# Kernel optimization log

Hardware: AMD Instinct MI355X
Metric: run time of the kernel (lower is better)

The kernel has to match this reference:

```python
import jax, jax.numpy as jnp
import numpy as np

T, D, H, V, Z = 32, 128, 256, 32000, 256


def _gru_cell(x, h, W_ih, W_hh, b_ih, b_hh):
    # PyTorch GRU cell, gate order r,z,n. x,h: [D,H]
    gi = x @ W_ih.T + b_ih
    gh = h @ W_hh.T + b_hh
    i_r, i_z, i_n = jnp.split(gi, 3, axis=-1)
    h_r, h_z, h_n = jnp.split(gh, 3, axis=-1)
    r = jax.nn.sigmoid(i_r + h_r)
    z = jax.nn.sigmoid(i_z + h_z)
    n = jnp.tanh(i_n + r * h_n)
    return (1.0 - z) * n + z * h


def _tree_rnn(nodes, edges, h0, emb, pc, ps):
    # nodes/edges: [T,D]; h0: [D,H]. Child vs sibling GRU chosen per-node by edges.
    def step(h, te):
        tok, e = te
        x = emb[tok]                       # [D,H]
        hc = _gru_cell(x, h, *pc)
        hs = _gru_cell(x, h, *ps)
        hn = jnp.where(e[:, None], hc, hs)  # branch-aware state update
        return hn, hn                       # seq_len=1, L=1 => output == new state
    h_final, outs = jax.lax.scan(step, h0, (nodes, edges))
    return outs, h_final                    # outs: [T,D,H]


def setup_inputs() -> dict:
    key = jax.random.key(0)
    ks = iter(jax.random.split(key, 48))
    s = 0.05
    def gru():
        return (jax.random.normal(next(ks), (3 * H, H), jnp.float32) * s,
                jax.random.normal(next(ks), (3 * H, H), jnp.float32) * s,
                jnp.zeros((3 * H,), jnp.float32),
                jnp.zeros((3 * H,), jnp.float32))
    inp = {}
    inp['nodes'] = jax.random.randint(next(ks), (T, D), 0, V, dtype=jnp.int32)
    inp['edges'] = jax.random.bernoulli(next(ks), 0.5, (T, D))
    inp['emb'] = jax.random.normal(next(ks), (V, H), jnp.float32) * s
    (inp['enc_c_Wih'], inp['enc_c_Whh'], inp['enc_c_bih'], inp['enc_c_bhh']) = gru()
    (inp['enc_s_Wih'], inp['enc_s_Whh'], inp['enc_s_bih'], inp['enc_s_bhh']) = gru()
    (inp['dec_c_Wih'], inp['dec_c_Whh'], inp['dec_c_bih'], inp['dec_c_bhh']) = gru()
    (inp['dec_s_Wih'], inp['dec_s_Whh'], inp['dec_s_bih'], inp['dec_s_bhh']) = gru()
    inp['W_mean'] = jax.random.normal(next(ks), (Z, H), jnp.float32) * s
    inp['b_mean'] = jnp.zeros((Z,), jnp.float32)
    inp['W_logv'] = jax.random.normal(next(ks), (Z, H), jnp.float32) * s
    inp['b_logv'] = jnp.zeros((Z,), jnp.float32)
    inp['W_l2h'] = jax.random.normal(next(ks), (H, Z), jnp.float32) * s
    inp['b_l2h'] = jnp.zeros((H,), jnp.float32)
    inp['W_out'] = jax.random.normal(next(ks), (V, H), jnp.float32) * s
    inp['b_out'] = jnp.zeros((V,), jnp.float32)
    inp['enc_init'] = jax.random.normal(next(ks), (D, H), jnp.float32) * 0.001
    inp['eps'] = jax.random.normal(next(ks), (D, Z), jnp.float32)
    return inp


def reference(nodes, edges, emb,
              enc_c_Wih, enc_c_Whh, enc_c_bih, enc_c_bhh,
              enc_s_Wih, enc_s_Whh, enc_s_bih, enc_s_bhh,
              dec_c_Wih, dec_c_Whh, dec_c_bih, dec_c_bhh,
              dec_s_Wih, dec_s_Whh, dec_s_bih, dec_s_bhh,
              W_mean, b_mean, W_logv, b_logv, W_l2h, b_l2h,
              W_out, b_out, enc_init, eps):
    pc_e = (enc_c_Wih, enc_c_Whh, enc_c_bih, enc_c_bhh)
    ps_e = (enc_s_Wih, enc_s_Whh, enc_s_bih, enc_s_bhh)
    pc_d = (dec_c_Wih, dec_c_Whh, dec_c_bih, dec_c_bhh)
    ps_d = (dec_s_Wih, dec_s_Whh, dec_s_bih, dec_s_bhh)

    _, hid = _tree_rnn(nodes, edges, enc_init, emb, pc_e, ps_e)  # [D,H]
    mean = hid @ W_mean.T + b_mean                               # [D,Z]
    logv = hid @ W_logv.T + b_logv
    z = eps * jnp.exp(0.5 * logv) + mean                          # reparameterize
    h0 = z @ W_l2h.T + b_l2h                                      # [D,H]
    outs, _ = _tree_rnn(nodes, edges, h0, emb, pc_d, ps_d)        # [T,D,H]
    logits = outs @ W_out.T + b_out                               # [T,D,V]
    logp = jax.nn.log_softmax(logits, axis=-1)
    return logp, mean, logv, z
```

## Files before the change

kernel.cpp:

```cpp
#include <hip/hip_runtime.h>
#include <hip/hip_bf16.h>

#define TT 32
#define DD 128
#define HH 256
#define VV 32000
#define ZZ 256
#define NTL 50
#define NBLK 16
#define GHLP 100

typedef __attribute__((ext_vector_type(8))) short bf16x8;
typedef __attribute__((ext_vector_type(4))) float f32x4;
typedef __attribute__((ext_vector_type(8))) _Float16 f16x8;

static __device__ inline unsigned short f2bf(float x) {
    __hip_bfloat16 h = __float2bfloat16(x);
    return *(unsigned short*)&h;
}

static __device__ inline unsigned long long pack4h(_Float16 a, _Float16 b,
                                                   _Float16 c, _Float16 d) {
    union { _Float16 h[4]; unsigned long long u; } x;
    x.h[0] = a; x.h[1] = b; x.h[2] = c; x.h[3] = d;
    return x.u;
}

__global__ void edge_canon_k(const unsigned char* __restrict__ eb,
                             unsigned char* __restrict__ canon)
{
    __shared__ int flag;
    if (threadIdx.x == 0) flag = 0;
    __syncthreads();
    int acc = 0;
    for (int i = threadIdx.x; i < TT * DD; i += 256)
        if (i & 3) acc |= eb[i];
    if (acc) atomicOr(&flag, 1);
    __syncthreads();
    const bool is_i32 = (flag == 0);
    for (int i = threadIdx.x; i < TT * DD; i += 256)
        canon[i] = is_i32 ? eb[4 * (size_t)i] : eb[i];
}

__global__ __launch_bounds__(256) void pack_frag(
    const float* __restrict__ src, __hip_bfloat16* __restrict__ dst, int nchunks_total)
{
    int i = blockIdx.x * 256 + threadIdx.x;
    if (i >= nchunks_total) return;
    int lane = i & 63, ks = (i >> 6) & 7, j = i >> 9;
    int g = lane >> 4, c = lane & 15;
    const float* s = src + (size_t)(j * 16 + c) * HH + ks * 32 + g * 8;
    float4 v0 = *(const float4*)s;
    float4 v1 = *(const float4*)(s + 4);
    bf16x8 o;
    o[0] = (short)f2bf(v0.x); o[1] = (short)f2bf(v0.y);
    o[2] = (short)f2bf(v0.z); o[3] = (short)f2bf(v0.w);
    o[4] = (short)f2bf(v1.x); o[5] = (short)f2bf(v1.y);
    o[6] = (short)f2bf(v1.z); o[7] = (short)f2bf(v1.w);
    *(bf16x8*)(dst + (size_t)i * 8) = o;
}

__global__ __launch_bounds__(256) void pack_frag4(
    const float* __restrict__ s0, const float* __restrict__ s1,
    const float* __restrict__ s2, const float* __restrict__ s3,
    __hip_bfloat16* __restrict__ dst)
{
    int i = blockIdx.x * 256 + threadIdx.x;
    if (i >= 24576) return;
    int slot = blockIdx.y;
    const float* src = (slot == 0) ? s0 : (slot == 1) ? s1 : (slot == 2) ? s2 : s3;
    __hip_bfloat16* d = dst + (size_t)slot * 196608;
    int lane = i & 63, ks = (i >> 6) & 7, j = i >> 9;
    int g = lane >> 4, c = lane & 15;
    const float* s = src + (size_t)(j * 16 + c) * HH + ks * 32 + g * 8;
    float4 v0 = *(const float4*)s;
    float4 v1 = *(const float4*)(s + 4);
    bf16x8 o;
    o[0] = (short)f2bf(v0.x); o[1] = (short)f2bf(v0.y);
    o[2] = (short)f2bf(v0.z); o[3] = (short)f2bf(v0.w);
    o[4] = (short)f2bf(v1.x); o[5] = (short)f2bf(v1.y);
    o[6] = (short)f2bf(v1.z); o[7] = (short)f2bf(v1.w);
    *(bf16x8*)(d + (size_t)i * 8) = o;
}

__global__ __launch_bounds__(256) void pack_wrnn4(
    const float* __restrict__ s0, const float* __restrict__ s1,
    const float* __restrict__ s2, const float* __restrict__ s3,
    _Float16* __restrict__ dst)
{
    int i = blockIdx.x * 256 + threadIdx.x;
    if (i >= 24576) return;
    int slot = blockIdx.y;
    const float* src = (slot == 0) ? s0 : (slot == 1) ? s1 : (slot == 2) ? s2 : s3;
    _Float16* d = dst + (size_t)slot * 196608;
    int lane = i & 63;
    int t2 = i >> 6;
    int ks = t2 & 7;
    int t3 = t2 >> 3;
    int tt = t3 % 6;
    int j8 = t3 / 6;
    int g = lane >> 4, c = lane & 15;
    int jg2 = tt / 3, gt = tt % 3;
    int srow = gt * 256 + j8 * 32 + jg2 * 16 + c;
    int scol = ks * 32 + g * 8;
    const float* s = src + (size_t)srow * HH + scol;
    float4 v0 = *(const float4*)s;
    float4 v1 = *(const float4*)(s + 4);
    f16x8 o;
    o[0] = (_Float16)v0.x; o[1] = (_Float16)v0.y;
    o[2] = (_Float16)v0.z; o[3] = (_Float16)v0.w;
    o[4] = (_Float16)v1.x; o[5] = (_Float16)v1.y;
    o[6] = (_Float16)v1.z; o[7] = (_Float16)v1.w;
    *(f16x8*)(d + (size_t)i * 8) = o;
}

__global__ __launch_bounds__(256) void gather_pack(
    const int* __restrict__ nodes, const float* __restrict__ emb,
    __hip_bfloat16* __restrict__ dst)
{
    int i = blockIdx.x * 256 + threadIdx.x;
    int lane = i & 63, ks = (i >> 6) & 7, j = i >> 9;
    int g = lane >> 4, c = lane & 15;
    int row = j * 16 + c;
    int tok = nodes[row];
    const float* s = emb + (size_t)tok * HH + ks * 32 + g * 8;
    float4 v0 = *(const float4*)s;
    float4 v1 = *(const float4*)(s + 4);
    bf16x8 o;
    o[0] = (short)f2bf(v0.x); o[1] = (short)f2bf(v0.y);
    o[2] = (short)f2bf(v0.z); o[3] = (short)f2bf(v0.w);
    o[4] = (short)f2bf(v1.x); o[5] = (short)f2bf(v1.y);
    o[6] = (short)f2bf(v1.z); o[7] = (short)f2bf(v1.w);
    *(bf16x8*)(dst + (size_t)i * 8) = o;
}

__global__ __launch_bounds__(256) void pack_lat3(
    const float* __restrict__ s0, const float* __restrict__ s1,
    const float* __restrict__ s2, float* __restrict__ dst)
{
    int i = blockIdx.x * 256 + threadIdx.x;
    int slot = blockIdx.y;
    const float* src = (slot == 0) ? s0 : (slot == 1) ? s1 : s2;
    float* d = dst + (size_t)slot * 65536;
    int j = i & 255, k = i >> 8;
    d[(size_t)k * 256 + j] = src[(size_t)j * 256 + k];
}

template<int MT, bool WRITE_C, bool HAS_BIAS, bool LSE_PARTIAL, bool LSE_SUB>
__global__ __launch_bounds__(256, 2) void gemm_rs(
    const __hip_bfloat16* __restrict__ A,
    const __hip_bfloat16* __restrict__ B,
    int ldc, int nchunks, int ntiles,
    const float* __restrict__ bias,
    const float* __restrict__ lse,
    float* __restrict__ C,
    float* __restrict__ pm, float* __restrict__ ps)
{
    __shared__ float lds_st[WRITE_C ? (4 * 16 * 68) : 1];

    const int tid  = threadIdx.x;
    const int w    = tid >> 6;
    const int lane = tid & 63;
    const int g    = lane >> 4;
    const int c    = lane & 15;
    const int m0   = blockIdx.x * (64 * MT);
    const int n0   = blockIdx.y * (nchunks * 64);
    const int jb0  = n0 >> 4;

    bf16x8 a[MT][8];
#pragma unroll
    for (int mt = 0; mt < MT; ++mt) {
        const int row16 = m0 + mt * 64 + w * 16;
        const __hip_bfloat16* ap = A + (((size_t)(row16 >> 4) * 8) * 64 + lane) * 8;
#pragma unroll
        for (int ks = 0; ks < 8; ++ks) a[mt][ks] = *(const bf16x8*)(ap + ks * 512);
    }

    float mrun[MT][4], srun[MT][4];
#pragma unroll
    for (int mt = 0; mt < MT; ++mt)
#pragma unroll
        for (int r = 0; r < 4; ++r) { mrun[mt][r] = -3.0e38f; srun[mt][r] = 0.f; }

    float lsev[MT][4];
    if (LSE_SUB) {
#pragma unroll
        for (int mt = 0; mt < MT; ++mt)
#pragma unroll
            for (int r = 0; r < 4; ++r)
                lsev[mt][r] = lse[m0 + mt * 64 + w * 16 + 4 * g + r];
    }

    for (int nc = 0; nc < nchunks; ++nc) {
        const int nb = n0 + nc * 64;
        const __hip_bfloat16* bp = B + (((size_t)(jb0 + nc * 4) * 8) * 64 + lane) * 8;

        f32x4 acc[MT][4];
#pragma unroll
        for (int mt = 0; mt < MT; ++mt)
#pragma unroll
            for (int nf = 0; nf < 4; ++nf) acc[mt][nf] = (f32x4){0.f, 0.f, 0.f, 0.f};

#pragma unroll
        for (int ks = 0; ks < 8; ++ks) {
            bf16x8 b0 = *(const bf16x8*)(bp + (0 * 8 + ks) * 512);
            bf16x8 b1 = *(const bf16x8*)(bp + (1 * 8 + ks) * 512);
            bf16x8 b2 = *(const bf16x8*)(bp + (2 * 8 + ks) * 512);
            bf16x8 b3 = *(const bf16x8*)(bp + (3 * 8 + ks) * 512);
#pragma unroll
            for (int mt = 0; mt < MT; ++mt) {
                acc[mt][0] = __builtin_amdgcn_mfma_f32_16x16x32_bf16(a[mt][ks], b0, acc[mt][0], 0, 0, 0);
                acc[mt][1] = __builtin_amdgcn_mfma_f32_16x16x32_bf16(a[mt][ks], b1, acc[mt][1], 0, 0, 0);
                acc[mt][2] = __builtin_amdgcn_mfma_f32_16x16x32_bf16(a[mt][ks], b2, acc[mt][2], 0, 0, 0);
                acc[mt][3] = __builtin_amdgcn_mfma_f32_16x16x32_bf16(a[mt][ks], b3, acc[mt][3], 0, 0, 0);
            }
        }

        float bv[4] = {0.f, 0.f, 0.f, 0.f};
        if (HAS_BIAS) {
#pragma unroll
            for (int nf = 0; nf < 4; ++nf) bv[nf] = bias[nb + nf * 16 + c];
        }

        if (LSE_PARTIAL) {
#pragma unroll
            for (int mt = 0; mt < MT; ++mt)
#pragma unroll
                for (int r = 0; r < 4; ++r) {
                    float l0 = acc[mt][0][r] + bv[0];
                    float l1 = acc[mt][1][r] + bv[1];
                    float l2 = acc[mt][2][r] + bv[2];
                    float l3 = acc[mt][3][r] + bv[3];
                    float mc = fmaxf(fmaxf(l0, l1), fmaxf(l2, l3));
                    float mn = fmaxf(mrun[mt][r], mc);
                    srun[mt][r] = srun[mt][r] * __expf(mrun[mt][r] - mn)
                            + __expf(l0 - mn) + __expf(l1 - mn)
                            + __expf(l2 - mn) + __expf(l3 - mn);
                    mrun[mt][r] = mn;
                }
        }

        if (WRITE_C) {
            const int base = w * (16 * 68);
#pragma unroll
            for (int mt = 0; mt < MT; ++mt) {
                const int row16 = m0 + mt * 64 + w * 16;
#pragma unroll
                for (int nf = 0; nf < 4; ++nf)
#pragma unroll
                    for (int r = 0; r < 4; ++r) {
                        float v = acc[mt][nf][r] + bv[nf];
                        if (LSE_SUB) v -= lsev[mt][r];
                        lds_st[base + (4 * g + r) * 68 + nf * 16 + c] = v;
                    }
#pragma unroll
                for (int i = 0; i < 4; ++i) {
                    int lr = i * 4 + g;
                    float4 v = *(const float4*)&lds_st[base + lr * 68 + c * 4];
                    *(float4*)(C + (size_t)(row16 + lr) * ldc + nb + c * 4) = v;
                }
            }
        }
    }

    if (LSE_PARTIAL) {
#pragma unroll
        for (int mt = 0; mt < MT; ++mt)
#pragma unroll
            for (int r = 0; r < 4; ++r) {
                float m = mrun[mt][r], s = srun[mt][r];
#pragma unroll
                for (int mk = 1; mk <= 8; mk <<= 1) {
                    float m2 = __shfl_xor(m, mk);
                    float s2 = __shfl_xor(s, mk);
                    float mn = fmaxf(m, m2);
                    s = s * __expf(m - mn) + s2 * __expf(m2 - mn);
                    m = mn;
                }
                if (c == 0) {
                    int row = m0 + mt * 64 + w * 16 + 4 * g + r;
                    pm[(size_t)row * ntiles + blockIdx.y] = m;
                    ps[(size_t)row * ntiles + blockIdx.y] = s;
                }
            }
    }
}

__global__ __launch_bounds__(512) void rnn_fused6(
    const unsigned char* __restrict__ ecan,
    const float* __restrict__ gi,
    const _Float16* __restrict__ Wr,
    const float* __restrict__ ecbih, const float* __restrict__ ecbhh,
    const float* __restrict__ esbih, const float* __restrict__ esbhh,
    const float* __restrict__ dcbih, const float* __restrict__ dcbhh,
    const float* __restrict__ dsbih, const float* __restrict__ dsbhh,
    const float* __restrict__ WmT, const float* __restrict__ WlT,
    const float* __restrict__ WhT,
    const float* __restrict__ b_mean, const float* __restrict__ b_logv,
    const float* __restrict__ b_l2h,
    const float* __restrict__ enc_init, const float* __restrict__ eps,
    float* __restrict__ out_mean, float* __restrict__ out_logv,
    float* __restrict__ out_z,
    __hip_bfloat16* __restrict__ outs_pk,
    _Float16* __restrict__ xh,
    int* __restrict__ flags)
{
    __shared__ _Float16 wlds[6 * 8 * 64 * 8];
    __shared__ _Float16 hpk[64 * 64 * 8];
    __shared__ _Float16 ghl[DD * GHLP];
    __shared__ float    bsum[4 * 256];
    __shared__ unsigned char ecan_l[TT * DD];

    const int v   = blockIdx.x & 1;
    const int j8  = blockIdx.x >> 1;
    const int tid = threadIdx.x;
    const int w    = tid >> 6;
    const int lane = tid & 63;
    const int g    = lane >> 4;
    const int c    = lane & 15;
    const int dq   = w & 3;
    const int jg2  = w >> 2;

    for (int u = tid; u < TT * DD; u += 512) ecan_l[u] = ecan[u];

    for (int u = tid; u < 4096; u += 512) {
        int chunk = u >> 6, ln = u & 63;
        int dt = chunk >> 3, ks = chunk & 7, lg = ln >> 4, lc = ln & 15;
        const float* s = enc_init + (size_t)(dt * 16 + lc) * HH + ks * 32 + lg * 8;
        float4 v0 = *(const float4*)s;
        float4 v1 = *(const float4*)(s + 4);
        f16x8 o;
        o[0] = (_Float16)v0.x; o[1] = (_Float16)v0.y;
        o[2] = (_Float16)v0.z; o[3] = (_Float16)v0.w;
        o[4] = (_Float16)v1.x; o[5] = (_Float16)v1.y;
        o[6] = (_Float16)v1.z; o[7] = (_Float16)v1.w;
        *(f16x8*)&hpk[(size_t)u * 8] = o;
    }
    __syncthreads();

    int bi = 0;

    for (int p = 0; p < 2; ++p) {
        {
            const _Float16* wsrc = Wr + ((size_t)(p * 2 + v) * 8 + j8) * (3072 * 8);
            for (int idx = tid; idx < 3072; idx += 512)
                *(f16x8*)&wlds[(size_t)idx * 8] = *(const f16x8*)(wsrc + (size_t)idx * 8);
        }
        {
            const float* bih = p ? (v ? dsbih : dcbih) : (v ? esbih : ecbih);
            const float* bhh = p ? (v ? dsbhh : dcbhh) : (v ? esbhh : ecbhh);
            if (tid < 256) {
                bsum[tid]       = bih[tid]       + bhh[tid];
                bsum[256 + tid] = bih[256 + tid] + bhh[256 + tid];
                bsum[512 + tid] = bih[512 + tid];
                bsum[768 + tid] = bhh[512 + tid];
            }
        }
        __syncthreads();

        for (int st = 0; st < TT; ++st) {
            f32x4 gpr0[3], gpr1[3];
            bool sel0, sel1;
            {
                const int u0 = tid, u1 = tid + 512;
                const int d0 = u0 >> 3, d1 = u1 >> 3;
                const int jgA = j8 * 32 + (u0 & 7) * 4;
                const int jgB = j8 * 32 + (u1 & 7) * 4;
                sel0 = (ecan_l[st * DD + d0] != 0) == (v == 0);
                sel1 = (ecan_l[st * DD + d1] != 0) == (v == 0);
                if (sel0) {
                    const float* gp = gi + (size_t)(st * DD + d0) * 3072 + p * 1536 + v * 768 + jgA;
                    gpr0[0] = *(const f32x4*)gp;
                    gpr0[1] = *(const f32x4*)(gp + 256);
                    gpr0[2] = *(const f32x4*)(gp + 512);
                }
                if (sel1) {
                    const float* gp = gi + (size_t)(st * DD + d1) * 3072 + p * 1536 + v * 768 + jgB;
                    gpr1[0] = *(const f32x4*)gp;
                    gpr1[1] = *(const f32x4*)(gp + 256);
                    gpr1[2] = *(const f32x4*)(gp + 512);
                }
            }

            f32x4 acc[2][3];
#pragma unroll
            for (int a = 0; a < 2; ++a)
#pragma unroll
                for (int b = 0; b < 3; ++b) acc[a][b] = (f32x4){0.f, 0.f, 0.f, 0.f};
#pragma unroll
            for (int ks = 0; ks < 8; ++ks) {
                f16x8 a0 = *(const f16x8*)&hpk[(((dq * 2 + 0) * 8 + ks) * 64 + lane) * 8];
                f16x8 a1 = *(const f16x8*)&hpk[(((dq * 2 + 1) * 8 + ks) * 64 + lane) * 8];
#pragma unroll
                for (int gt = 0; gt < 3; ++gt) {
                    f16x8 bf = *(const f16x8*)&wlds[(((jg2 * 3 + gt) * 8 + ks) * 64 + lane) * 8];
                    acc[0][gt] = __builtin_amdgcn_mfma_f32_16x16x32_f16(a0, bf, acc[0][gt], 0, 0, 0);
                    acc[1][gt] = __builtin_amdgcn_mfma_f32_16x16x32_f16(a1, bf, acc[1][gt], 0, 0, 0);
                }
            }

#pragma unroll
            for (int dti = 0; dti < 2; ++dti) {
                const int dt = dq * 2 + dti;
#pragma unroll
                for (int gt = 0; gt < 3; ++gt)
#pragma unroll
                    for (int rr = 0; rr < 4; ++rr)
                        ghl[(dt * 16 + 4 * g + rr) * GHLP + gt * 32 + jg2 * 16 + c] =
                            (_Float16)acc[dti][gt][rr];
            }
            __syncthreads();

            _Float16* xcur = xh + (size_t)bi * (DD * HH);
#pragma unroll
            for (int uu = 0; uu < 2; ++uu) {
                const bool sel = uu ? sel1 : sel0;
                if (!sel) continue;
                const int u = tid + uu * 512;
                const int d = u >> 3, jq = u & 7;
                const int jl = jq * 4;
                const int jg_ = j8 * 32 + jl;
                const f32x4* gpr = uu ? gpr1 : gpr0;

                f32x4 br  = *(const f32x4*)&bsum[jg_];
                f32x4 bz  = *(const f32x4*)&bsum[256 + jg_];
                f32x4 bni = *(const f32x4*)&bsum[512 + jg_];
                f32x4 bnh = *(const f32x4*)&bsum[768 + jg_];
                const _Float16* gd = &ghl[d * GHLP];
                const int dt = d >> 4, lc = d & 15, ks = jg_ >> 5, lg = (jg_ >> 3) & 3;
                const int ch = ((dt * 8 + ks) * 64 + lg * 16 + lc);
                const _Float16* hop = &hpk[(size_t)ch * 8 + (jg_ & 7)];

                _Float16 hn[4];
                unsigned short ob[4];
#pragma unroll
                for (int m = 0; m < 4; ++m) {
                    float ghr = (float)gd[jl + m];
                    float ghz = (float)gd[32 + jl + m];
                    float ghn = (float)gd[64 + jl + m];
                    float rg = 1.f / (1.f + __expf(-(gpr[0][m] + br[m] + ghr)));
                    float zg = 1.f / (1.f + __expf(-(gpr[1][m] + bz[m] + ghz)));
                    float nn = tanhf(gpr[2][m] + bni[m] + rg * (ghn + bnh[m]));
                    float hv = (1.f - zg) * nn + zg * (float)hop[m];
                    hn[m] = (_Float16)hv;
                    ob[m] = f2bf(hv);
                }
                __hip_atomic_store((unsigned long long*)(xcur + (size_t)d * HH + jg_),
                                   pack4h(hn[0], hn[1], hn[2], hn[3]),
                                   __ATOMIC_RELAXED, __HIP_MEMORY_SCOPE_AGENT);
                if (p) {
                    union { unsigned short s[4]; unsigned long long u; } ou;
                    ou.s[0] = ob[0]; ou.s[1] = ob[1]; ou.s[2] = ob[2]; ou.s[3] = ob[3];
                    size_t och = ((size_t)(st * 8 + dt) * 8 + ks) * 64 + lg * 16 + lc;
                    *(unsigned long long*)((unsigned short*)outs_pk + och * 8 + (jg_ & 7)) = ou.u;
                }
            }
            __syncthreads();

            if (tid == 0)
                __hip_atomic_store(&flags[blockIdx.x], bi + 1,
                                   __ATOMIC_RELAXED, __HIP_MEMORY_SCOPE_AGENT);
            if (tid < 64) {
                for (;;) {
                    int f = (tid < NBLK)
                          ? __hip_atomic_load(&flags[tid], __ATOMIC_RELAXED, __HIP_MEMORY_SCOPE_AGENT)
                          : 0x7fffffff;
                    if (__all(f >= bi + 1)) break;
                    __builtin_amdgcn_s_sleep(1);
                }
            }
            __syncthreads();

            {
                const _Float16* xr = xh + (size_t)bi * (DD * HH);
                f16x8 tv[8];
#pragma unroll
                for (int i = 0; i < 8; ++i) {
                    int u = tid + i * 512;
                    int chunk = u >> 6, ln = u & 63;
                    int dt = chunk >> 3, ks = chunk & 7, lg = ln >> 4, lc = ln & 15;
                    tv[i] = *(const f16x8*)(xr + (size_t)(dt * 16 + lc) * HH + ks * 32 + lg * 8);
                }
#pragma unroll
                for (int i = 0; i < 8; ++i)
                    *(f16x8*)&hpk[(size_t)(tid + i * 512) * 8] = tv[i];
            }
            __syncthreads();
            ++bi;
        }

        if (p == 0) {
            float* hlin = (float*)ghl;
            const int d8 = tid >> 6;
            const int q  = tid & 63;
            const int dg = blockIdx.x * 8 + d8;
            for (int u = tid; u < 2048; u += 512) {
                int du = u >> 8, k = u & 255;
                int d = blockIdx.x * 8 + du;
                hlin[du * 256 + k] = (float)hpk[(((size_t)(d >> 4) * 8 + (k >> 5)) * 64
                                      + ((k >> 3) & 3) * 16 + (d & 15)) * 8 + (k & 7)];
            }
            __syncthreads();
            f32x4 mean4, logv4;
            {
                f32x4 sm = {0, 0, 0, 0}, sl = {0, 0, 0, 0};
                const float* hl = hlin + d8 * 256;
                for (int k = 0; k < HH; ++k) {
                    float hv = hl[k];
                    sm += hv * *(const f32x4*)(WmT + (size_t)k * 256 + q * 4);
                    sl += hv * *(const f32x4*)(WlT + (size_t)k * 256 + q * 4);
                }
                mean4 = sm + *(const f32x4*)(b_mean + q * 4);
                logv4 = sl + *(const f32x4*)(b_logv + q * 4);
                *(f32x4*)(out_mean + (size_t)dg * ZZ + q * 4) = mean4;
                *(f32x4*)(out_logv + (size_t)dg * ZZ + q * 4) = logv4;
            }
            __syncthreads();
            {
                f32x4 ep = *(const f32x4*)(eps + (size_t)dg * ZZ + q * 4);
                f32x4 zv;
#pragma unroll
                for (int m = 0; m < 4; ++m)
                    zv[m] = ep[m] * __expf(0.5f * logv4[m]) + mean4[m];
                *(f32x4*)(out_z + (size_t)dg * ZZ + q * 4) = zv;
                *(f32x4*)(hlin + d8 * 256 + q * 4) = zv;
            }
            __syncthreads();
            {
                f32x4 s = {0, 0, 0, 0};
                const float* zlp = hlin + d8 * 256;
                for (int k = 0; k < ZZ; ++k)
                    s += zlp[k] * *(const f32x4*)(WhT + (size_t)k * 256 + q * 4);
                f32x4 h0v = s + *(const f32x4*)(b_l2h + q * 4);
                __hip_atomic_store(
                    (unsigned long long*)(xh + (size_t)bi * (DD * HH) + (size_t)dg * HH + q * 4),
                    pack4h((_Float16)h0v[0], (_Float16)h0v[1],
                           (_Float16)h0v[2], (_Float16)h0v[3]),
                    __ATOMIC_RELAXED, __HIP_MEMORY_SCOPE_AGENT);
            }
            __syncthreads();
            if (tid == 0)
                __hip_atomic_store(&flags[blockIdx.x], bi + 1,
                                   __ATOMIC_RELAXED, __HIP_MEMORY_SCOPE_AGENT);
            if (tid < 64) {
                for (;;) {
                    int f = (tid < NBLK)
                          ? __hip_atomic_load(&flags[tid], __ATOMIC_RELAXED, __HIP_MEMORY_SCOPE_AGENT)
                          : 0x7fffffff;
                    if (__all(f >= bi + 1)) break;
                    __builtin_amdgcn_s_sleep(1);
                }
            }
            __syncthreads();
            {
                const _Float16* xr = xh + (size_t)bi * (DD * HH);
                f16x8 tv[8];
#pragma unroll
                for (int i = 0; i < 8; ++i) {
                    int u = tid + i * 512;
                    int chunk = u >> 6, ln = u & 63;
                    int dt = chunk >> 3, ks = chunk & 7, lg = ln >> 4, lc = ln & 15;
                    tv[i] = *(const f16x8*)(xr + (size_t)(dt * 16 + lc) * HH + ks * 32 + lg * 8);
                }
#pragma unroll
                for (int i = 0; i < 8; ++i)
                    *(f16x8*)&hpk[(size_t)(tid + i * 512) * 8] = tv[i];
            }
            __syncthreads();
            ++bi;
        }
    }
}

__global__ __launch_bounds__(64) void lse_reduce(
    const float* __restrict__ pm, const float* __restrict__ ps,
    float* __restrict__ lse, int nt)
{
    int row = blockIdx.x;
    int l = threadIdx.x;
    float m = (l < nt) ? pm[(size_t)row * nt + l] : -3.0e38f;
    float s = (l < nt) ? ps[(size_t)row * nt + l] : 0.f;
    for (int mk = 1; mk <= 32; mk <<= 1) {
        float m2 = __shfl_xor(m, mk);
        float s2 = __shfl_xor(s, mk);
        float mn = fmaxf(m, m2);
        s = s * __expf(m - mn) + s2 * __expf(m2 - mn);
        m = mn;
    }
    if (l == 0) lse[row] = m + logf(s);
}

extern "C" void kernel_launch(void* const* d_in, const int* in_sizes, int n_in,
                              void* d_out, int out_size, void* d_ws, size_t ws_size,
                              hipStream_t stream)
{
    const int*           nodes     = (const int*)d_in[0];
    const unsigned char* edges_raw = (const unsigned char*)d_in[1];
    const float* emb    = (const float*)d_in[2];
    const float* ecWih  = (const float*)d_in[3];
    const float* ecWhh  = (const float*)d_in[4];
    const float* ecbih  = (const float*)d_in[5];
    const float* ecbhh  = (const float*)d_in[6];
    const float* esWih  = (const float*)d_in[7];
    const float* esWhh  = (const float*)d_in[8];
    const float* esbih  = (const float*)d_in[9];
    const float* esbhh  = (const float*)d_in[10];
    const float* dcWih  = (const float*)d_in[11];
    const float* dcWhh  = (const float*)d_in[12];
    const float* dcbih  = (const float*)d_in[13];
    const float* dcbhh  = (const float*)d_in[14];
    const float* dsWih  = (const float*)d_in[15];
    const float* dsWhh  = (const float*)d_in[16];
    const float* dsbih  = (const float*)d_in[17];
    const float* dsbhh  = (const float*)d_in[18];
    const float* W_mean = (const float*)d_in[19];
    const float* b_mean = (const float*)d_in[20];
    const float* W_logv = (const float*)d_in[21];
    const float* b_logv = (const float*)d_in[22];
    const float* W_l2h  = (const float*)d_in[23];
    const float* b_l2h  = (const float*)d_in[24];
    const float* W_out  = (const float*)d_in[25];
    const float* b_out  = (const float*)d_in[26];
    const float* enc_init = (const float*)d_in[27];
    const float* eps    = (const float*)d_in[28];

    float* out      = (float*)d_out;
    float* out_mean = out + (size_t)TT * DD * VV;
    float* out_logv = out_mean + DD * ZZ;
    float* out_z    = out_logv + DD * ZZ;
    float* gi       = out;

    char* ws = (char*)d_ws;
    __hip_bfloat16* outs_pk = (__hip_bfloat16*)(ws + 0);
    __hip_bfloat16* Ap      = (__hip_bfloat16*)(ws + 2097152);
    __hip_bfloat16* Wp      = (__hip_bfloat16*)(ws + 4194304);
    __hip_bfloat16* Bp_all  = (__hip_bfloat16*)(ws + 20971520);
    _Float16*       Wr      = (_Float16*)(ws + 22544384);
    float*          WmT     = (float*)(ws + 24117248);
    float*          pm      = (float*)(ws + 24903680);
    float*          ps      = (float*)(ws + 25722880);
    float*          lse     = (float*)(ws + 26542080);
    unsigned char*  ecan    = (unsigned char*)(ws + 26558464);
    _Float16*       xh      = (_Float16*)(ws + 26562560);
    int*            flags   = (int*)(ws + 30822400);
    float*          WlT     = WmT + 65536;
    float*          WhT     = WmT + 131072;

    hipMemsetAsync(flags, 0, 64, stream);

    edge_canon_k<<<1, 256, 0, stream>>>(edges_raw, ecan);
    pack_frag<<<4000, 256, 0, stream>>>(W_out, Wp, 2000 * 8 * 64);
    pack_frag4<<<dim3(96, 4), 256, 0, stream>>>(ecWih, esWih, dcWih, dsWih, Bp_all);
    pack_wrnn4<<<dim3(96, 4), 256, 0, stream>>>(ecWhh, esWhh, dcWhh, dsWhh, Wr);
    pack_lat3<<<dim3(256, 3), 256, 0, stream>>>(W_mean, W_logv, W_l2h, WmT);
    gather_pack<<<512, 256, 0, stream>>>(nodes, emb, Ap);

    gemm_rs<2, true, false, false, false><<<dim3(32, 6), 256, 0, stream>>>(
        Ap, Bp_all, 3072, 8, 6, nullptr, nullptr, gi, nullptr, nullptr);

    rnn_fused6<<<NBLK, 512, 0, stream>>>(
        ecan, gi, Wr,
        ecbih, ecbhh, esbih, esbhh, dcbih, dcbhh, dsbih, dsbhh,
        WmT, WlT, WhT, b_mean, b_logv, b_l2h,
        enc_init, eps, out_mean, out_logv, out_z, outs_pk, xh, flags);

    gemm_rs<2, false, true, true, false><<<dim3(32, NTL), 256, 0, stream>>>(
        outs_pk, Wp, VV, 10, NTL, b_out, nullptr, nullptr, pm, ps);
    lse_reduce<<<4096, 64, 0, stream>>>(pm, ps, lse, NTL);
    gemm_rs<2, true, true, false, true><<<dim3(32, NTL), 256, 0, stream>>>(
        outs_pk, Wp, VV, 10, NTL, b_out, lse, out, nullptr, nullptr);
}
```

Before: 902.7 us.

## Stage output-projection B tiles into LDS with double-buffered async global loads

Adds a new GEMM variant for the vocab projection that loads each B tile straight into LDS through the global-to-LDS load builtin, double-buffered so the next tile's fetch overlaps the current tile's MFMAs. Both the LSE-partial pass and the final log-softmax write pass now use it. The goal is to hide global-load latency for the large W_out stream and share each B tile across all four waves. In exchange it uses 64KB of LDS per block and adds a block barrier per chunk, which may limit occupancy.

Measured after the change: 811.0 us. 1.11x faster.

```diff
diff --git a/kernel.cpp b/kernel.cpp
--- a/kernel.cpp
+++ b/kernel.cpp
@@ -24,6 +24,12 @@
     union { _Float16 h[4]; unsigned long long u; } x;
     x.h[0] = a; x.h[1] = b; x.h[2] = c; x.h[3] = d;
     return x.u;
+}
+
+static __device__ inline void gload_lds16(const void* g, void* l) {
+    __builtin_amdgcn_global_load_lds(
+        (const __attribute__((address_space(1))) void*)g,
+        (__attribute__((address_space(3))) void*)l, 16, 0, 0);
 }
 
 __global__ void edge_canon_k(const unsigned char* __restrict__ eb,
@@ -266,6 +272,167 @@
     if (LSE_PARTIAL) {
 #pragma unroll
         for (int mt = 0; mt < MT; ++mt)
+#pragma unroll
+            for (int r = 0; r < 4; ++r) {
+                float m = mrun[mt][r], s = srun[mt][r];
+#pragma unroll
+                for (int mk = 1; mk <= 8; mk <<= 1) {
+                    float m2 = __shfl_xor(m, mk);
+                    float s2 = __shfl_xor(s, mk);
+                    float mn = fmaxf(m, m2);
+                    s = s * __expf(m - mn) + s2 * __expf(m2 - mn);
+                    m = mn;
+                }
+                if (c == 0) {
+                    int row = m0 + mt * 64 + w * 16 + 4 * g + r;
+                    pm[(size_t)row * ntiles + blockIdx.y] = m;
+                    ps[(size_t)row * ntiles + blockIdx.y] = s;
+                }
+            }
+    }
+}
+
+template<bool WRITE_C, bool HAS_BIAS, bool LSE_PARTIAL, bool LSE_SUB>
+__global__ __launch_bounds__(256, 2) void gemm_ls(
+    const __hip_bfloat16* __restrict__ A,
+    const __hip_bfloat16* __restrict__ B,
+    int ldc, int nchunks, int ntiles,
+    const float* __restrict__ bias,
+    const float* __restrict__ lse,
+    float* __restrict__ C,
+    float* __restrict__ pm, float* __restrict__ ps)
+{
+    __shared__ __align__(16) char ldsB[2][32768];
+    __shared__ float lds_st[WRITE_C ? (4 * 16 * 68) : 1];
+
+    const int tid  = threadIdx.x;
+    const int w    = tid >> 6;
+    const int lane = tid & 63;
+    const int g    = lane >> 4;
+    const int c    = lane & 15;
+    const int m0   = blockIdx.x * 128;
+    const int n0   = blockIdx.y * (nchunks * 64);
+    const int jb0  = n0 >> 4;
+
+    bf16x8 a[2][8];
+#pragma unroll
+    for (int mt = 0; mt < 2; ++mt) {
+        const int row16 = m0 + mt * 64 + w * 16;
+        const __hip_bfloat16* ap = A + (((size_t)(row16 >> 4) * 8) * 64 + lane) * 8;
+#pragma unroll
+        for (int ks = 0; ks < 8; ++ks) a[mt][ks] = *(const bf16x8*)(ap + ks * 512);
+    }
+
+    float mrun[2][4], srun[2][4];
+#pragma unroll
+    for (int mt = 0; mt < 2; ++mt)
+#pragma unroll
+        for (int r = 0; r < 4; ++r) { mrun[mt][r] = -3.0e38f; srun[mt][r] = 0.f; }
+
+    float lsev[2][4];
+    if (LSE_SUB) {
+#pragma unroll
+        for (int mt = 0; mt < 2; ++mt)
+#pragma unroll
+            for (int r = 0; r < 4; ++r)
+                lsev[mt][r] = lse[m0 + mt * 64 + w * 16 + 4 * g + r];
+    }
+
+    const char* Bbase = (const char*)B;
+#define STAGE_TILE(bbuf, nc_)                                                     \
+    {                                                                             \
+        const char* src = Bbase + ((size_t)(jb0 + (nc_) * 4) * 8 * 64) * 16;      \
+        _Pragma("unroll")                                                         \
+        for (int i_ = 0; i_ < 8; ++i_) {                                          \
+            int seg = w * 8 + i_;                                                 \
+            gload_lds16(src + (size_t)seg * 1024 + lane * 16,                     \
+                        &ldsB[bbuf][seg * 1024]);                                 \
+        }                                                                         \
+    }
+
+    int buf = 0;
+    STAGE_TILE(0, 0);
+    __syncthreads();
+
+    for (int nc = 0; nc < nchunks; ++nc) {
+        if (nc + 1 < nchunks) STAGE_TILE(buf ^ 1, nc + 1);
+
+        const int nb = n0 + nc * 64;
+        f32x4 acc[2][4];
+#pragma unroll
+        for (int mt = 0; mt < 2; ++mt)
+#pragma unroll
+            for (int nf = 0; nf < 4; ++nf) acc[mt][nf] = (f32x4){0.f, 0.f, 0.f, 0.f};
+
+#pragma unroll
+        for (int ks = 0; ks < 8; ++ks) {
+            bf16x8 b0 = *(const bf16x8*)&ldsB[buf][((0 * 8 + ks) * 64 + lane) * 16];
+            bf16x8 b1 = *(const bf16x8*)&ldsB[buf][((1 * 8 + ks) * 64 + lane) * 16];
+            bf16x8 b2 = *(const bf16x8*)&ldsB[buf][((2 * 8 + ks) * 64 + lane) * 16];
+            bf16x8 b3 = *(const bf16x8*)&ldsB[buf][((3 * 8 + ks) * 64 + lane) * 16];
+#pragma unroll
+            for (int mt = 0; mt < 2; ++mt) {
+                acc[mt][0] = __builtin_amdgcn_mfma_f32_16x16x32_bf16(a[mt][ks], b0, acc[mt][0], 0, 0, 0);
+                acc[mt][1] = __builtin_amdgcn_mfma_f32_16x16x32_bf16(a[mt][ks], b1, acc[mt][1], 0, 0, 0);
+                acc[mt][2] = __builtin_amdgcn_mfma_f32_16x16x32_bf16(a[mt][ks], b2, acc[mt][2], 0, 0, 0);
+                acc[mt][3] = __builtin_amdgcn_mfma_f32_16x16x32_bf16(a[mt][ks], b3, acc[mt][3], 0, 0, 0);
+            }
+        }
+
+        float bv[4] = {0.f, 0.f, 0.f, 0.f};
+        if (HAS_BIAS) {
+#pragma unroll
+            for (int nf = 0; nf < 4; ++nf) bv[nf] = bias[nb + nf * 16 + c];
+        }
+
+        if (LSE_PARTIAL) {
+#pragma unroll
+            for (int mt = 0; mt < 2; ++mt)
+#pragma unroll
+                for (int r = 0; r < 4; ++r) {
+                    float l0 = acc[mt][0][r] + bv[0];
+                    float l1 = acc[mt][1][r] + bv[1];
+                    float l2 = acc[mt][2][r] + bv[2];
+                    float l3 = acc[mt][3][r] + bv[3];
+                    float mc = fmaxf(fmaxf(l0, l1), fmaxf(l2, l3));
+                    float mn = fmaxf(mrun[mt][r], mc);
+                    srun[mt][r] = srun[mt][r] * __expf(mrun[mt][r] - mn)
+                            + __expf(l0 - mn) + __expf(l1 - mn)
+                            + __expf(l2 - mn) + __expf(l3 - mn);
+                    mrun[mt][r] = mn;
+                }
+        }
+
+        if (WRITE_C) {
+            const int base = w * (16 * 68);
+#pragma unroll
+            for (int mt = 0; mt < 2; ++mt) {
+                const int row16 = m0 + mt * 64 + w * 16;
+#pragma unroll
+                for (int nf = 0; nf < 4; ++nf)
+#pragma unroll
+                    for (int r = 0; r < 4; ++r) {
+                        float v = acc[mt][nf][r] + bv[nf];
+                        if (LSE_SUB) v -= lsev[mt][r];
+                        lds_st[base + (4 * g + r) * 68 + nf * 16 + c] = v;
+                    }
+#pragma unroll
+                for (int i = 0; i < 4; ++i) {
+                    int lr = i * 4 + g;
+                    float4 v = *(const float4*)&lds_st[base + lr * 68 + c * 4];
+                    *(float4*)(C + (size_t)(row16 + lr) * ldc + nb + c * 4) = v;
+                }
+            }
+        }
+
+        __syncthreads();
+        buf ^= 1;
+    }
+#undef STAGE_TILE
+
+    if (LSE_PARTIAL) {
+#pragma unroll
+        for (int mt = 0; mt < 2; ++mt)
 #pragma unroll
             for (int r = 0; r < 4; ++r) {
                 float m = mrun[mt][r], s = srun[mt][r];
@@ -664,9 +831,9 @@
         WmT, WlT, WhT, b_mean, b_logv, b_l2h,
         enc_init, eps, out_mean, out_logv, out_z, outs_pk, xh, flags);
 
-    gemm_rs<2, false, true, true, false><<<dim3(32, NTL), 256, 0, stream>>>(
+    gemm_ls<false, true, true, false><<<dim3(32, NTL), 256, 0, stream>>>(
         outs_pk, Wp, VV, 10, NTL, b_out, nullptr, nullptr, pm, ps);
     lse_reduce<<<4096, 64, 0, stream>>>(pm, ps, lse, NTL);
-    gemm_rs<2, true, true, false, true><<<dim3(32, NTL), 256, 0, stream>>>(
+    gemm_ls<true, true, false, true><<<dim3(32, NTL), 256, 0, stream>>>(
         outs_pk, Wp, VV, 10, NTL, b_out, lse, out, nullptr, nullptr);
 }
```
